# Kernel tuning notes

Measured on AMD Instinct MI355X. Metric: run time of the kernel, lower is better.

Reference implementation:

```python
import jax, jax.numpy as jnp
import numpy as np

DOMAIN_MIN, DOMAIN_MAX = -1.0, 1.0
N, D_IN, D_OUT, K = 1024, 128, 128, 8


def setup_inputs() -> dict:
    key = jax.random.key(0)
    k1, k2, k3 = jax.random.split(key, 3)
    x = jax.random.uniform(k1, (N, D_IN), dtype=jnp.float32,
                           minval=DOMAIN_MIN, maxval=DOMAIN_MAX)
    # Per-edge spline knot values: near-identity init plus small noise.
    base = jnp.linspace(DOMAIN_MIN, DOMAIN_MAX, K, dtype=jnp.float32)
    coeffs = base[None, None, :] + 0.1 * jax.random.normal(
        k2, (D_OUT, D_IN, K), dtype=jnp.float32)
    weights = jax.random.normal(k3, (D_OUT, D_IN), dtype=jnp.float32) * np.sqrt(2.0 / D_IN)
    bias = jnp.zeros((D_OUT,), dtype=jnp.float32)
    return {"x": x, "coeffs": coeffs, "weights": weights, "bias": bias}


def _spline_all_edges(x, coeffs):
    """Evaluate every edge's cubic (Catmull-Rom) spline at its input.
    x: [N, d_in]; coeffs: [d_out, d_in, K] knot values on uniform knots in [-1,1].
    Returns s: [N, d_in, d_out]."""
    K_ = coeffs.shape[-1]
    h = (DOMAIN_MAX - DOMAIN_MIN) / (K_ - 1)
    xc = jnp.clip(x, DOMAIN_MIN, DOMAIN_MAX)
    t = (xc - DOMAIN_MIN) / h                      # [N, d_in], in [0, K-1]
    idx = jnp.clip(jnp.floor(t).astype(jnp.int32), 0, K_ - 2)
    u = t - idx                                    # local coord in [0,1]
    i0 = jnp.clip(idx - 1, 0, K_ - 1)
    i1 = idx
    i2 = idx + 1
    i3 = jnp.clip(idx + 2, 0, K_ - 1)
    ct = jnp.transpose(coeffs, (1, 2, 0))          # [d_in, K, d_out]
    jar = jnp.arange(ct.shape[0])[None, :]          # [1, d_in]
    p0 = ct[jar, i0]                               # [N, d_in, d_out]
    p1 = ct[jar, i1]
    p2 = ct[jar, i2]
    p3 = ct[jar, i3]
    u2 = u * u
    u3 = u2 * u
    b0 = 0.5 * (-u3 + 2.0 * u2 - u)
    b1 = 0.5 * (3.0 * u3 - 5.0 * u2 + 2.0)
    b2 = 0.5 * (-3.0 * u3 + 4.0 * u2 + u)
    b3 = 0.5 * (u3 - u2)
    return (b0[..., None] * p0 + b1[..., None] * p1 +
            b2[..., None] * p2 + b3[..., None] * p3)


def reference(x, coeffs, weights, bias):
    # h_i(x) = sum_j w_ij * s_ij(x_j) + b_i
    s = _spline_all_edges(x, coeffs)               # [N, d_in, d_out]
    return jnp.einsum('njo,oj->no', s, weights) + bias[None, :]
```

## Files before the change

### kernel.cpp

```cpp
#include <hip/hip_runtime.h>
#include <hip/hip_bf16.h>
#include <stdint.h>


#define DIN 128
#define DOUT 128
#define KK 8
#define KTOT 1024
#define MT 16
#define OT 16
#define KC 256
#define JC 32
#define SW 264

typedef unsigned int u32;
typedef unsigned short u16;
typedef __attribute__((ext_vector_type(8))) short bf16x8;
typedef __attribute__((ext_vector_type(4))) float f32x4;

union H8 { u16 s[8]; uint4 v; };

__device__ __forceinline__ u16 f2b(float f) {
    __hip_bfloat16 h = __float2bfloat16(f);
    union { __hip_bfloat16 h; u16 u; } c; c.h = h; return c.u;
}

__global__ __launch_bounds__(256) void kan_mfma(
    const float* __restrict__ x, const float* __restrict__ coeffs,
    const float* __restrict__ weights, const float* __restrict__ bias,
    float* __restrict__ out)
{
    __shared__ __align__(16) u16 sA[MT * SW];
    __shared__ __align__(16) u16 sB[OT * SW];
    __shared__ float sC[4 * MT * OT];

    const int tid  = threadIdx.x;
    const int wave = tid >> 6;
    const int lane = tid & 63;
    const int n0 = blockIdx.x * MT;
    const int o0 = blockIdx.y * OT;

    const int m = lane & 15;
    const int q = lane >> 4;

    f32x4 acc = {0.0f, 0.0f, 0.0f, 0.0f};

    for (int ch = 0; ch < 4; ++ch) {
        #pragma unroll
        for (int i = 0; i < 4; ++i) {
            const int ol = i * 4 + wave;
            const int kc = lane * 4;
            const int kg = ch * KC + kc;
            const float4 c4 = *(const float4*)(coeffs + (o0 + ol) * KTOT + kg);
            const float wv = weights[(o0 + ol) * DIN + (kg >> 3)];
            ushort4 b;
            b.x = f2b(c4.x * wv); b.y = f2b(c4.y * wv);
            b.z = f2b(c4.z * wv); b.w = f2b(c4.w * wv);
            *(ushort4*)(sB + ol * SW + kc) = b;
        }

        #pragma unroll
        for (int it = 0; it < 2; ++it) {
            const int task = tid + it * 256;
            const int row = task >> 5;
            const int jl = task & 31;
            const int j = ch * JC + jl;
            float xv = x[(n0 + row) * DIN + j];
            xv = fminf(fmaxf(xv, -1.0f), 1.0f);
            const float t = (xv + 1.0f) * 3.5f;
            int idx = (int)t; idx = idx > 6 ? 6 : idx;
            const float u = t - (float)idx;
            const float u2 = u * u, u3 = u2 * u;
            const float b0 = 0.5f * (-u3 + 2.0f * u2 - u);
            const float b1 = 0.5f * (3.0f * u3 - 5.0f * u2 + 2.0f);
            const float b2 = 0.5f * (-3.0f * u3 + 4.0f * u2 + u);
            const float b3 = 0.5f * (u3 - u2);
            float r[8];
            #pragma unroll
            for (int k = 0; k < 8; ++k) r[k] = 0.0f;
            int i0 = idx - 1; i0 = i0 < 0 ? 0 : i0;
            int i3 = idx + 2; i3 = i3 > 7 ? 7 : i3;
            r[i0] += b0; r[idx] += b1; r[idx + 1] += b2; r[i3] += b3;
            H8 h;
            #pragma unroll
            for (int k = 0; k < 8; ++k) h.s[k] = f2b(r[k]);
            *(uint4*)(sA + row * SW + jl * 8) = h.v;
        }
        __syncthreads();

        const int kq = wave * 64;
        #pragma unroll
        for (int s = 0; s < 2; ++s) {
            const int kk = kq + s * 32 + q * 8;
            bf16x8 af = *(const bf16x8*)(sA + m * SW + kk);
            bf16x8 bf = *(const bf16x8*)(sB + m * SW + kk);
            acc = __builtin_amdgcn_mfma_f32_16x16x32_bf16(af, bf, acc, 0, 0, 0);
        }
        __syncthreads();
    }

    #pragma unroll
    for (int r = 0; r < 4; ++r) {
        const int row = q * 4 + r;
        sC[wave * (MT * OT) + row * OT + m] = acc[r];
    }
    __syncthreads();
    const int orow = tid >> 4;
    const int ocol = tid & 15;
    float v = sC[tid] + sC[256 + tid] + sC[512 + tid] + sC[768 + tid];
    v += bias[o0 + ocol];
    out[(n0 + orow) * DOUT + o0 + ocol] = v;
}

extern "C" void kernel_launch(void* const* d_in, const int* in_sizes, int n_in,
                              void* d_out, int out_size, void* d_ws, size_t ws_size,
                              hipStream_t stream) {
    const float* x       = (const float*)d_in[0];
    const float* coeffs  = (const float*)d_in[1];
    const float* weights = (const float*)d_in[2];
    const float* bias    = (const float*)d_in[3];
    float* out = (float*)d_out;
    const int N = in_sizes[0] / DIN;
    dim3 grid(N / MT, DOUT / OT);
    kan_mfma<<<grid, 256, 0, stream>>>(x, coeffs, weights, bias, out);
}
```

Before: 65.32 us.

## Build full spline basis tile once and stream weighted coeffs directly into MFMA registers

The whole 16x1024 basis tile of sparse cubic weights is now built in shared memory once, instead of in four chunked stages with a sync pair each. The B operand (coeff*weight) is loaded straight from global memory into registers per MFMA step, with no staging through LDS. Each block now covers 32 outputs, with waves split across two output tiles and two K halves, which halves the grid. This removes most barriers and LDS traffic for B. In exchange the block needs a larger LDS footprint and a zero-fill pass, and the global coefficient loads sit on the MFMA critical path.

```diff
diff --git a/kernel.cpp b/kernel.cpp
--- a/kernel.cpp
+++ b/kernel.cpp
@@ -5,24 +5,19 @@
 
 #define DIN 128
 #define DOUT 128
-#define KK 8
 #define KTOT 1024
 #define MT 16
-#define OT 16
-#define KC 256
-#define JC 32
-#define SW 264
+#define PADW 1032
 
 typedef unsigned int u32;
 typedef unsigned short u16;
 typedef __attribute__((ext_vector_type(8))) short bf16x8;
 typedef __attribute__((ext_vector_type(4))) float f32x4;
 
-union H8 { u16 s[8]; uint4 v; };
-
 __device__ __forceinline__ u16 f2b(float f) {
-    __hip_bfloat16 h = __float2bfloat16(f);
-    union { __hip_bfloat16 h; u16 u; } c; c.h = h; return c.u;
+    union { __hip_bfloat16 h; u16 u; } c;
+    c.h = __float2bfloat16(f);
+    return c.u;
 }
 
 __global__ __launch_bounds__(256) void kan_mfma(
@@ -30,86 +25,88 @@
     const float* __restrict__ weights, const float* __restrict__ bias,
     float* __restrict__ out)
 {
-    __shared__ __align__(16) u16 sA[MT * SW];
-    __shared__ __align__(16) u16 sB[OT * SW];
-    __shared__ float sC[4 * MT * OT];
+    __shared__ __align__(16) u16 sA[MT * PADW];
+    __shared__ float sC[4 * 256];
 
     const int tid  = threadIdx.x;
     const int wave = tid >> 6;
     const int lane = tid & 63;
     const int n0 = blockIdx.x * MT;
-    const int o0 = blockIdx.y * OT;
+    const int og = blockIdx.y * 32;
 
-    const int m = lane & 15;
-    const int q = lane >> 4;
+    #pragma unroll
+    for (int it = 0; it < 8; ++it) {
+        const int z = tid + it * 256;
+        const int row = z >> 7, c16 = z & 127;
+        *(uint4*)(sA + row * PADW + c16 * 8) = uint4{0u, 0u, 0u, 0u};
+    }
+    __syncthreads();
+
+    #pragma unroll
+    for (int it = 0; it < 8; ++it) {
+        const int task = tid + it * 256;
+        const int row = task >> 7;
+        const int j = task & 127;
+        float xv = x[(n0 + row) * DIN + j];
+        xv = fminf(fmaxf(xv, -1.0f), 1.0f);
+        const float t = (xv + 1.0f) * 3.5f;
+        int idx = (int)t; idx = idx > 6 ? 6 : idx;
+        const float u = t - (float)idx;
+        const float u2 = u * u, u3 = u2 * u;
+        const float b0 = 0.5f * (-u3 + 2.0f * u2 - u);
+        const float b1 = 0.5f * (3.0f * u3 - 5.0f * u2 + 2.0f);
+        const float b2 = 0.5f * (-3.0f * u3 + 4.0f * u2 + u);
+        const float b3 = 0.5f * (u3 - u2);
+        u16* r = sA + row * PADW + j * 8;
+        const int i0 = idx > 0 ? idx - 1 : 0;
+        const int i3 = idx < 6 ? idx + 2 : 7;
+        r[idx]     = f2b(b1);
+        r[idx + 1] = f2b(b2);
+        r[i0]      = f2b(idx == 0 ? b0 + b1 : b0);
+        r[i3]      = f2b(idx == 6 ? b2 + b3 : b3);
+    }
+    __syncthreads();
+
+    const int ot = wave & 1;
+    const int kh = wave >> 1;
+    const int mo = lane & 15;
+    const int q  = lane >> 4;
+
+    const int orow = og + ot * 16 + mo;
+    const float* cp = coeffs + orow * KTOT + kh * 512 + q * 8;
+    const float* wp = weights + orow * DIN + kh * 64 + q;
+    const u16*   ap = sA + mo * PADW + kh * 512 + q * 8;
 
     f32x4 acc = {0.0f, 0.0f, 0.0f, 0.0f};
-
-    for (int ch = 0; ch < 4; ++ch) {
-        #pragma unroll
-        for (int i = 0; i < 4; ++i) {
-            const int ol = i * 4 + wave;
-            const int kc = lane * 4;
-            const int kg = ch * KC + kc;
-            const float4 c4 = *(const float4*)(coeffs + (o0 + ol) * KTOT + kg);
-            const float wv = weights[(o0 + ol) * DIN + (kg >> 3)];
-            ushort4 b;
-            b.x = f2b(c4.x * wv); b.y = f2b(c4.y * wv);
-            b.z = f2b(c4.z * wv); b.w = f2b(c4.w * wv);
-            *(ushort4*)(sB + ol * SW + kc) = b;
-        }
-
-        #pragma unroll
-        for (int it = 0; it < 2; ++it) {
-            const int task = tid + it * 256;
-            const int row = task >> 5;
-            const int jl = task & 31;
-            const int j = ch * JC + jl;
-            float xv = x[(n0 + row) * DIN + j];
-            xv = fminf(fmaxf(xv, -1.0f), 1.0f);
-            const float t = (xv + 1.0f) * 3.5f;
-            int idx = (int)t; idx = idx > 6 ? 6 : idx;
-            const float u = t - (float)idx;
-            const float u2 = u * u, u3 = u2 * u;
-            const float b0 = 0.5f * (-u3 + 2.0f * u2 - u);
-            const float b1 = 0.5f * (3.0f * u3 - 5.0f * u2 + 2.0f);
-            const float b2 = 0.5f * (-3.0f * u3 + 4.0f * u2 + u);
-            const float b3 = 0.5f * (u3 - u2);
-            float r[8];
-            #pragma unroll
-            for (int k = 0; k < 8; ++k) r[k] = 0.0f;
-            int i0 = idx - 1; i0 = i0 < 0 ? 0 : i0;
-            int i3 = idx + 2; i3 = i3 > 7 ? 7 : i3;
-            r[i0] += b0; r[idx] += b1; r[idx + 1] += b2; r[i3] += b3;
-            H8 h;
-            #pragma unroll
-            for (int k = 0; k < 8; ++k) h.s[k] = f2b(r[k]);
-            *(uint4*)(sA + row * SW + jl * 8) = h.v;
-        }
-        __syncthreads();
-
-        const int kq = wave * 64;
-        #pragma unroll
-        for (int s = 0; s < 2; ++s) {
-            const int kk = kq + s * 32 + q * 8;
-            bf16x8 af = *(const bf16x8*)(sA + m * SW + kk);
-            bf16x8 bf = *(const bf16x8*)(sB + m * SW + kk);
-            acc = __builtin_amdgcn_mfma_f32_16x16x32_bf16(af, bf, acc, 0, 0, 0);
-        }
-        __syncthreads();
+    #pragma unroll 4
+    for (int s = 0; s < 16; ++s) {
+        bf16x8 af = *(const bf16x8*)(ap + s * 32);
+        const float4 c0 = *(const float4*)(cp + s * 32);
+        const float4 c1 = *(const float4*)(cp + s * 32 + 4);
+        const float wv = wp[s * 4];
+        bf16x8 bfr;
+        bfr[0] = (short)f2b(c0.x * wv); bfr[1] = (short)f2b(c0.y * wv);
+        bfr[2] = (short)f2b(c0.z * wv); bfr[3] = (short)f2b(c0.w * wv);
+        bfr[4] = (short)f2b(c1.x * wv); bfr[5] = (short)f2b(c1.y * wv);
+        bfr[6] = (short)f2b(c1.z * wv); bfr[7] = (short)f2b(c1.w * wv);
+        acc = __builtin_amdgcn_mfma_f32_16x16x32_bf16(af, bfr, acc, 0, 0, 0);
     }
 
     #pragma unroll
-    for (int r = 0; r < 4; ++r) {
-        const int row = q * 4 + r;
-        sC[wave * (MT * OT) + row * OT + m] = acc[r];
+    for (int r = 0; r < 4; ++r)
+        sC[wave * 256 + (q * 4 + r) * 16 + mo] = acc[r];
+    __syncthreads();
+
+    #pragma unroll
+    for (int t2 = 0; t2 < 2; ++t2) {
+        const int e = tid + t2 * 256;
+        const int tile = e >> 8;
+        const int idx = e & 255;
+        const int row = idx >> 4, col = idx & 15;
+        float v = sC[tile * 256 + idx] + sC[(tile + 2) * 256 + idx];
+        const int oc = og + tile * 16 + col;
+        out[(n0 + row) * DOUT + oc] = v + bias[oc];
     }
-    __syncthreads();
-    const int orow = tid >> 4;
-    const int ocol = tid & 15;
-    float v = sC[tid] + sC[256 + tid] + sC[512 + tid] + sC[768 + tid];
-    v += bias[o0 + ocol];
-    out[(n0 + orow) * DOUT + o0 + ocol] = v;
 }
 
 extern "C" void kernel_launch(void* const* d_in, const int* in_sizes, int n_in,
@@ -121,6 +118,6 @@
     const float* bias    = (const float*)d_in[3];
     float* out = (float*)d_out;
     const int N = in_sizes[0] / DIN;
-    dim3 grid(N / MT, DOUT / OT);
+    dim3 grid(N / MT, DOUT / 32);
     kan_mfma<<<grid, 256, 0, stream>>>(x, coeffs, weights, bias, out);
 }
```

Measured after the change: 65.12 us. About the same (-0.3%).
